# Kernel tuning notes

Measured on AMD Instinct MI355X. Metric: run time of the kernel, lower is better.

The kernel has to match this reference:

```python
import jax, jax.numpy as jnp
import numpy as np

MARGIN = 1.0
EPS = 1e-08


def setup_inputs() -> dict:
    key = jax.random.key(0)
    k0, k1 = jax.random.split(key)
    kernels0 = jax.random.normal(k0, (2048, 3, 3), dtype=jnp.float32)
    kernels1 = jax.random.normal(k1, (1024, 5, 5), dtype=jnp.float32)
    return {"kernels0": kernels0, "kernels1": kernels1}


def _layer_loss(kernels):
    n, d, _ = kernels.shape
    # Frobenius-normalize each kernel
    norms = jnp.sqrt(jnp.sum(kernels * kernels, axis=(1, 2), keepdims=True)) + EPS
    kn = kernels / norms                      # (n, d, d)
    inv = jnp.linalg.inv(kn)                  # (n, d, d)
    # AB[i, j] = inv[i] @ kn[j]; BA[i, j] = inv[j] @ kn[i]
    ab = jnp.einsum('iab,jbc->ijac', inv, kn)  # (n, n, d, d)
    ba = jnp.einsum('jab,ibc->ijac', inv, kn)  # (n, n, d, d)
    eye = jnp.eye(d, dtype=kernels.dtype)
    diff_ab = jnp.sqrt(jnp.sum((eye - ab) ** 2, axis=(2, 3)))  # (n, n)
    diff_ba = jnp.sqrt(jnp.sum((eye - ba) ** 2, axis=(2, 3)))  # (n, n)
    combined = jnp.tril(diff_ab) + jnp.triu(diff_ba)
    loss_mat = jax.nn.relu(MARGIN - combined)
    mask = ~jnp.eye(n, dtype=bool)
    loss_mat = jnp.where(mask, loss_mat, 0.0)
    return jnp.sum(loss_mat) / (n * (n - 1))


def reference(kernels0, kernels1):
    losses = [_layer_loss(kernels0), _layer_loss(kernels1)]
    return sum(losses) / len(losses)
```

## Files before the change

kernel.cpp:

```cpp
#include <hip/hip_runtime.h>
#include <math.h>

#define N0 2048
#define N1 1024
#define T0 128
#define T1 64
#define M0 (N0 / T0)
#define M1 (N1 / T1)
#define NB0 (M0 * (M0 + 1) / 2)
#define NB1 (M1 * (M1 + 1) / 2)
#define NBTOT (NB0 + NB1)


__global__ __launch_bounds__(64) void prep_kernel(const float* __restrict__ k0,
                                                  const float* __restrict__ k1,
                                                  float* __restrict__ kn0,
                                                  float* __restrict__ inv0,
                                                  float* __restrict__ kn1,
                                                  float* __restrict__ inv1) {
    int t = blockIdx.x * blockDim.x + threadIdx.x;
    if (t < N0) {
        float a[9];
        float ss = 0.0f;
#pragma unroll
        for (int e = 0; e < 9; ++e) { a[e] = k0[t * 9 + e]; ss = fmaf(a[e], a[e], ss); }
        float rn = 1.0f / (sqrtf(ss) + 1e-8f);
#pragma unroll
        for (int e = 0; e < 9; ++e) a[e] *= rn;
        float c00 = a[4] * a[8] - a[5] * a[7];
        float c01 = -(a[3] * a[8] - a[5] * a[6]);
        float c02 = a[3] * a[7] - a[4] * a[6];
        float det = a[0] * c00 + a[1] * c01 + a[2] * c02;
        float id = 1.0f / det;
        float x[9];
        x[0] = c00 * id;
        x[1] = (a[2] * a[7] - a[1] * a[8]) * id;
        x[2] = (a[1] * a[5] - a[2] * a[4]) * id;
        x[3] = c01 * id;
        x[4] = (a[0] * a[8] - a[2] * a[6]) * id;
        x[5] = (a[2] * a[3] - a[0] * a[5]) * id;
        x[6] = c02 * id;
        x[7] = (a[1] * a[6] - a[0] * a[7]) * id;
        x[8] = (a[0] * a[4] - a[1] * a[3]) * id;
        float r[9];
#pragma unroll
        for (int i = 0; i < 3; ++i)
#pragma unroll
            for (int j = 0; j < 3; ++j) {
                float m = a[i * 3 + 0] * x[j];
                m = fmaf(a[i * 3 + 1], x[3 + j], m);
                m = fmaf(a[i * 3 + 2], x[6 + j], m);
                r[i * 3 + j] = ((i == j) ? 2.0f : 0.0f) - m;
            }
#pragma unroll
        for (int i = 0; i < 3; ++i)
#pragma unroll
            for (int j = 0; j < 3; ++j) {
                float m = x[i * 3 + 0] * r[j];
                m = fmaf(x[i * 3 + 1], r[3 + j], m);
                m = fmaf(x[i * 3 + 2], r[6 + j], m);
                inv0[t * 9 + i * 3 + j] = m;
            }
#pragma unroll
        for (int e = 0; e < 9; ++e) kn0[t * 9 + e] = a[e];
    } else {
        int u = t - N0;
        if (u < N1) {
            float A[5][5], B[5][5], K[5][5];
            float ss = 0.0f;
#pragma unroll
            for (int r = 0; r < 5; ++r)
#pragma unroll
                for (int c = 0; c < 5; ++c) {
                    float v = k1[u * 25 + r * 5 + c];
                    A[r][c] = v;
                    ss = fmaf(v, v, ss);
                }
            float rn = 1.0f / (sqrtf(ss) + 1e-8f);
#pragma unroll
            for (int r = 0; r < 5; ++r)
#pragma unroll
                for (int c = 0; c < 5; ++c) {
                    A[r][c] *= rn;
                    K[r][c] = A[r][c];
                    kn1[u * 25 + r * 5 + c] = A[r][c];
                    B[r][c] = (r == c) ? 1.0f : 0.0f;
                }
#pragma unroll
            for (int k = 0; k < 5; ++k) {
#pragma unroll
                for (int r = k + 1; r < 5; ++r) {
                    bool sw = fabsf(A[r][k]) > fabsf(A[k][k]);
#pragma unroll
                    for (int c = k; c < 5; ++c) {
                        float Ar = A[r][c], Ak = A[k][c];
                        A[r][c] = sw ? Ak : Ar;
                        A[k][c] = sw ? Ar : Ak;
                    }
#pragma unroll
                    for (int c = 0; c < 5; ++c) {
                        float Br = B[r][c], Bk = B[k][c];
                        B[r][c] = sw ? Bk : Br;
                        B[k][c] = sw ? Br : Bk;
                    }
                }
                float piv = 1.0f / A[k][k];
#pragma unroll
                for (int c = k; c < 5; ++c) A[k][c] *= piv;
#pragma unroll
                for (int c = 0; c < 5; ++c) B[k][c] *= piv;
#pragma unroll
                for (int r = 0; r < 5; ++r) {
                    if (r == k) continue;
                    float f = A[r][k];
#pragma unroll
                    for (int c = k; c < 5; ++c) A[r][c] = fmaf(-f, A[k][c], A[r][c]);
#pragma unroll
                    for (int c = 0; c < 5; ++c) B[r][c] = fmaf(-f, B[k][c], B[r][c]);
                }
            }
            float R[5][5];
#pragma unroll
            for (int i = 0; i < 5; ++i)
#pragma unroll
                for (int j = 0; j < 5; ++j) {
                    float m = K[i][0] * B[0][j];
#pragma unroll
                    for (int k = 1; k < 5; ++k) m = fmaf(K[i][k], B[k][j], m);
                    R[i][j] = ((i == j) ? 2.0f : 0.0f) - m;
                }
#pragma unroll
            for (int i = 0; i < 5; ++i)
#pragma unroll
                for (int j = 0; j < 5; ++j) {
                    float m = B[i][0] * R[0][j];
#pragma unroll
                    for (int k = 1; k < 5; ++k) m = fmaf(B[i][k], R[k][j], m);
                    inv1[u * 25 + i * 5 + j] = m;
                }
        }
    }
}

__device__ __forceinline__ void tri_decode(int t, int& bi, int& bj) {
    bi = (int)((sqrtf(8.0f * t + 1.0f) - 1.0f) * 0.5f);
    while ((bi + 1) * (bi + 2) / 2 <= t) ++bi;
    while (bi * (bi + 1) / 2 > t) --bi;
    bj = t - bi * (bi + 1) / 2;
}

__global__ __launch_bounds__(256) void pairs_kernel(const float* __restrict__ inv0,
                                                    const float* __restrict__ kn0,
                                                    const float* __restrict__ inv1,
                                                    const float* __restrict__ kn1,
                                                    float* __restrict__ out) {
    __shared__ float sA[1600];
    __shared__ float sB[1600];
    int tid = threadIdx.x;
    float contrib = 0.0f;
    bool isL0 = blockIdx.x < NB0;

    if (isL0) {
        int bi, bj;
        tri_decode(blockIdx.x, bi, bj);
        for (int e = tid; e < T0 * 9; e += 256) {
            sA[e] = inv0[bi * (T0 * 9) + e];
            sB[e] = kn0[bj * (T0 * 9) + e];
        }
        __syncthreads();

        int ty = tid >> 4, tx = tid & 15;
        float a[8][9];
#pragma unroll
        for (int u = 0; u < 8; ++u)
#pragma unroll
            for (int e = 0; e < 9; ++e) a[u][e] = sA[(ty + 16 * u) * 9 + e];
#pragma unroll
        for (int v = 0; v < 8; ++v) {
            float b[9];
#pragma unroll
            for (int e = 0; e < 9; ++e) b[e] = sB[(tx + 16 * v) * 9 + e];
            int j = bj * T0 + tx + 16 * v;
#pragma unroll
            for (int u = 0; u < 8; ++u) {
                float s = 0.0f;
#pragma unroll
                for (int r = 0; r < 3; ++r)
#pragma unroll
                    for (int c = 0; c < 3; ++c) {
                        float m = a[u][r * 3 + 0] * b[c];
                        m = fmaf(a[u][r * 3 + 1], b[3 + c], m);
                        m = fmaf(a[u][r * 3 + 2], b[6 + c], m);
                        float d = ((r == c) ? 1.0f : 0.0f) - m;
                        s = fmaf(d, d, s);
                    }
                int i = bi * T0 + ty + 16 * u;
                bool take = (i > j) && (s < 1.0f);
                contrib += take ? (1.0f - sqrtf(s)) : 0.0f;
            }
        }
    } else {
        int bi, bj;
        tri_decode(blockIdx.x - NB0, bi, bj);
        for (int e = tid; e < T1 * 25; e += 256) {
            sA[e] = inv1[bi * (T1 * 25) + e];
            sB[e] = kn1[bj * (T1 * 25) + e];
        }
        __syncthreads();

        int ty = tid >> 4, tx = tid & 15;
        float a[4][25];
#pragma unroll
        for (int u = 0; u < 4; ++u)
#pragma unroll
            for (int e = 0; e < 25; ++e) a[u][e] = sA[(ty + 16 * u) * 25 + e];
#pragma unroll
        for (int v = 0; v < 4; ++v) {
            float b[25];
#pragma unroll
            for (int e = 0; e < 25; ++e) b[e] = sB[(tx + 16 * v) * 25 + e];
            int j = bj * T1 + tx + 16 * v;
#pragma unroll
            for (int u = 0; u < 4; ++u) {
                float s = 0.0f;
#pragma unroll
                for (int r = 0; r < 5; ++r)
#pragma unroll
                    for (int c = 0; c < 5; ++c) {
                        float m = a[u][r * 5 + 0] * b[c];
#pragma unroll
                        for (int k = 1; k < 5; ++k) m = fmaf(a[u][r * 5 + k], b[k * 5 + c], m);
                        float d = ((r == c) ? 1.0f : 0.0f) - m;
                        s = fmaf(d, d, s);
                    }
                int i = bi * T1 + ty + 16 * u;
                bool take = (i > j) && (s < 1.0f);
                contrib += take ? (1.0f - sqrtf(s)) : 0.0f;
            }
        }
    }

#pragma unroll
    for (int off = 32; off; off >>= 1) contrib += __shfl_down(contrib, off);
    __shared__ float wsum[4];
    if ((tid & 63) == 0) wsum[tid >> 6] = contrib;
    __syncthreads();
    if (tid == 0) {
        double part = (double)(wsum[0] + wsum[1] + wsum[2] + wsum[3]);
        double scale = isL0 ? 1.0 / ((double)N0 * (double)(N0 - 1))
                            : 1.0 / ((double)N1 * (double)(N1 - 1));
        unsafeAtomicAdd(out, (float)(part * scale));
    }
}

extern "C" void kernel_launch(void* const* d_in, const int* in_sizes, int n_in,
                              void* d_out, int out_size, void* d_ws, size_t ws_size,
                              hipStream_t stream) {
    const float* k0 = (const float*)d_in[0];
    const float* k1 = (const float*)d_in[1];
    float* out = (float*)d_out;

    float* ws = (float*)d_ws;
    float* kn0 = ws;
    float* inv0 = kn0 + N0 * 9;
    float* kn1 = inv0 + N0 * 9;
    float* inv1 = kn1 + N1 * 25;

    int totalPrep = N0 + N1;
    prep_kernel<<<(totalPrep + 63) / 64, 64, 0, stream>>>(k0, k1, kn0, inv0, kn1, inv1);

    pairs_kernel<<<NBTOT, 256, 0, stream>>>(inv0, kn0, inv1, kn1, out);
}
```

Before: 75.73 us.

## Halve pair tiles for more blocks and replace atomics with a partial-sum finalize

Tile sizes for both layers are halved, so the triangular block grid grows from roughly 272 blocks to about 1056. Each block now handles fewer pairs, which should fill all CUs and even out the tail. The per-block atomicAdd is replaced by writing per-block partial sums to workspace, and a single-block finalize kernel reduces them in double precision. This trades some register and shared-memory reuse, plus one extra kernel launch, for better parallelism and a deterministic reduction.

```diff
diff --git a/kernel.cpp b/kernel.cpp
--- a/kernel.cpp
+++ b/kernel.cpp
@@ -3,8 +3,8 @@
 
 #define N0 2048
 #define N1 1024
-#define T0 128
-#define T1 64
+#define T0 64
+#define T1 32
 #define M0 (N0 / T0)
 #define M1 (N1 / T1)
 #define NB0 (M0 * (M0 + 1) / 2)
@@ -153,9 +153,9 @@
                                                     const float* __restrict__ kn0,
                                                     const float* __restrict__ inv1,
                                                     const float* __restrict__ kn1,
-                                                    float* __restrict__ out) {
-    __shared__ float sA[1600];
-    __shared__ float sB[1600];
+                                                    float* __restrict__ partial) {
+    __shared__ float sA[800];
+    __shared__ float sB[800];
     int tid = threadIdx.x;
     float contrib = 0.0f;
     bool isL0 = blockIdx.x < NB0;
@@ -170,19 +170,19 @@
         __syncthreads();
 
         int ty = tid >> 4, tx = tid & 15;
-        float a[8][9];
-#pragma unroll
-        for (int u = 0; u < 8; ++u)
+        float a[4][9];
+#pragma unroll
+        for (int u = 0; u < 4; ++u)
 #pragma unroll
             for (int e = 0; e < 9; ++e) a[u][e] = sA[(ty + 16 * u) * 9 + e];
 #pragma unroll
-        for (int v = 0; v < 8; ++v) {
+        for (int v = 0; v < 4; ++v) {
             float b[9];
 #pragma unroll
             for (int e = 0; e < 9; ++e) b[e] = sB[(tx + 16 * v) * 9 + e];
             int j = bj * T0 + tx + 16 * v;
 #pragma unroll
-            for (int u = 0; u < 8; ++u) {
+            for (int u = 0; u < 4; ++u) {
                 float s = 0.0f;
 #pragma unroll
                 for (int r = 0; r < 3; ++r)
@@ -209,19 +209,19 @@
         __syncthreads();
 
         int ty = tid >> 4, tx = tid & 15;
-        float a[4][25];
-#pragma unroll
-        for (int u = 0; u < 4; ++u)
+        float a[2][25];
+#pragma unroll
+        for (int u = 0; u < 2; ++u)
 #pragma unroll
             for (int e = 0; e < 25; ++e) a[u][e] = sA[(ty + 16 * u) * 25 + e];
 #pragma unroll
-        for (int v = 0; v < 4; ++v) {
+        for (int v = 0; v < 2; ++v) {
             float b[25];
 #pragma unroll
             for (int e = 0; e < 25; ++e) b[e] = sB[(tx + 16 * v) * 25 + e];
             int j = bj * T1 + tx + 16 * v;
 #pragma unroll
-            for (int u = 0; u < 4; ++u) {
+            for (int u = 0; u < 2; ++u) {
                 float s = 0.0f;
 #pragma unroll
                 for (int r = 0; r < 5; ++r)
@@ -245,11 +245,28 @@
     __shared__ float wsum[4];
     if ((tid & 63) == 0) wsum[tid >> 6] = contrib;
     __syncthreads();
+    if (tid == 0) partial[blockIdx.x] = wsum[0] + wsum[1] + wsum[2] + wsum[3];
+}
+
+__global__ void finalize_kernel(const float* __restrict__ partial, float* __restrict__ out) {
+    int tid = threadIdx.x;
+    double s0 = 0.0, s1 = 0.0;
+    for (int x = tid; x < NB0; x += 256) s0 += (double)partial[x];
+    for (int x = NB0 + tid; x < NBTOT; x += 256) s1 += (double)partial[x];
+#pragma unroll
+    for (int off = 32; off; off >>= 1) {
+        s0 += __shfl_down(s0, off);
+        s1 += __shfl_down(s1, off);
+    }
+    __shared__ double w0[4], w1[4];
+    if ((tid & 63) == 0) { w0[tid >> 6] = s0; w1[tid >> 6] = s1; }
+    __syncthreads();
     if (tid == 0) {
-        double part = (double)(wsum[0] + wsum[1] + wsum[2] + wsum[3]);
-        double scale = isL0 ? 1.0 / ((double)N0 * (double)(N0 - 1))
-                            : 1.0 / ((double)N1 * (double)(N1 - 1));
-        unsafeAtomicAdd(out, (float)(part * scale));
+        double S0 = w0[0] + w0[1] + w0[2] + w0[3];
+        double S1 = w1[0] + w1[1] + w1[2] + w1[3];
+        double res = S0 / ((double)N0 * (double)(N0 - 1)) +
+                     S1 / ((double)N1 * (double)(N1 - 1));
+        out[0] = (float)res;
     }
 }
 
@@ -265,9 +282,12 @@
     float* inv0 = kn0 + N0 * 9;
     float* kn1 = inv0 + N0 * 9;
     float* inv1 = kn1 + N1 * 25;
+    float* partial = inv1 + N1 * 25;
 
     int totalPrep = N0 + N1;
     prep_kernel<<<(totalPrep + 63) / 64, 64, 0, stream>>>(k0, k1, kn0, inv0, kn1, inv1);
 
-    pairs_kernel<<<NBTOT, 256, 0, stream>>>(inv0, kn0, inv1, kn1, out);
-}
+    pairs_kernel<<<NBTOT, 256, 0, stream>>>(inv0, kn0, inv1, kn1, partial);
+
+    finalize_kernel<<<1, 256, 0, stream>>>(partial, out);
+}
```

Result: faster. 70.12 us (-7.4%).
